# Kernel tuning notes

Measured on AMD Instinct MI355X. Metric: run time of the kernel, lower is better.

## Reference

```python
import jax, jax.numpy as jnp
import numpy as np

LOSS_WEIGHT = 1.0
BIG = 1e9  # finite sentinel for masked-out pixels (avoids inf-grad NaNs)


def setup_inputs() -> dict:
    key = jax.random.key(0)
    k1, k2 = jax.random.split(key)
    B, N, H, W = 4, 6890, 64, 64
    vert2d = jax.random.uniform(k1, (B, N, 2), dtype=jnp.float32) * jnp.array([W, H], jnp.float32)
    mask = jax.random.randint(k2, (B, H, W), 0, 2, dtype=jnp.int32)
    return {"vert2d": vert2d, "mask": mask}


def reference(vert2d, mask):
    B, N, _ = vert2d.shape
    _, H, W = mask.shape
    scale = jnp.array([W, H], vert2d.dtype)
    v = vert2d / scale  # [B,N,2], normalized
    # all pixel coords as (x, y), normalized -- the dense equivalent of torch.where points
    ys, xs = jnp.meshgrid(jnp.arange(H), jnp.arange(W), indexing="ij")
    pts = (jnp.stack([xs.ravel(), ys.ravel()], axis=-1).astype(v.dtype) / scale)  # [HW,2]
    valid = (mask.reshape(B, -1) > 0)  # [B,HW] boolean membership of each pixel
    # pairwise L2 distances: [B,N,HW]
    diff = v[:, :, None, :] - pts[None, None, :, :]
    d = jnp.sqrt(jnp.sum(diff * diff, axis=-1))
    dm = jnp.where(valid[:, None, :], d, BIG)
    # sum over mask points of min over verts  +  sum over verts of min over mask points
    loss = jnp.sum(jnp.min(dm, axis=1) * valid) + jnp.sum(jnp.min(dm, axis=2))
    return LOSS_WEIGHT * loss
```

## Files before the change

### kernel.cpp

```cpp
#include <hip/hip_runtime.h>

#define NB 4
#define NV 6890
#define HW 4096
#define NV4 3445
#define CH4 108
#define CH4P 111
#define NCHUNK 32
#define T2_BPB 54
#define T2_BLOCKS (NB * T2_BPB)
#define T1_BLOCKS (NB * 64)
#define FINF 3.402823466e38f
#define VBIG 1.0e9f
#define PBIG 1.0e18f
#define INV_S (1.0f / 64.0f)

__global__ __launch_bounds__(256) void k_fused(const float* __restrict__ vert,
                                               const int* __restrict__ mask,
                                               float* __restrict__ out) {
    __shared__ __align__(16) char smem[65024];
    int bx = blockIdx.x, tid = threadIdx.x;
    if (bx < T2_BLOCKS) {
        float2* pt = reinterpret_cast<float2*>(smem);
        float*  pr = reinterpret_cast<float*>(smem + 32768);
        float*  sb = reinterpret_cast<float*>(smem + 34816);
        int b = bx / T2_BPB, blk = bx - b * T2_BPB;
        for (int i = tid; i < HW; i += 256) {
            int x = i & 63;
            float fx = (float)x;
            float e = (mask[b * HW + i] > 0) ? fx * fx : PBIG;
            pt[i] = make_float2(-2.f * fx, e);
        }
        int g = tid & 63, rq = tid >> 6;
        int n0 = blk * 128 + 2 * g;
        float4 vp = make_float4(0.f, 0.f, 0.f, 0.f);
        if (n0 < NV)
            vp = reinterpret_cast<const float4*>(vert)[(b * NV + n0) >> 1];
        __syncthreads();
        float vx0 = vp.x, vy0 = vp.y, vx1 = vp.z, vy1 = vp.w;
        float vx20 = vx0 * vx0, vx21 = vx1 * vx1;
        float m0 = FINF, m1 = FINF;
        float fy = (float)(rq * 16);
        for (int y = rq * 16; y < rq * 16 + 16; ++y, fy += 1.f) {
            const float4* row = reinterpret_cast<const float4*>(pt + y * 64);
            float r0 = FINF, r1 = FINF;
            #pragma unroll 8
            for (int j = 0; j < 32; ++j) {
                float4 a = row[j];
                r0 = fminf(r0, fminf(fmaf(a.x, vx0, a.y), fmaf(a.z, vx0, a.w)));
                r1 = fminf(r1, fminf(fmaf(a.x, vx1, a.y), fmaf(a.z, vx1, a.w)));
            }
            float t0 = vy0 - fy, t1 = vy1 - fy;
            m0 = fminf(m0, r0 + fmaf(t0, t0, vx20));
            m1 = fminf(m1, r1 + fmaf(t1, t1, vx21));
        }
        reinterpret_cast<float2*>(pr)[rq * 64 + g] = make_float2(m0, m1);
        __syncthreads();
        float s = 0.f;
        if (tid < 128) {
            float mm = fminf(fminf(pr[tid], pr[128 + tid]),
                             fminf(pr[256 + tid], pr[384 + tid]));
            if (blk * 128 + tid < NV) s = sqrtf(fmaxf(mm, 0.f));
        }
        #pragma unroll
        for (int off = 32; off; off >>= 1) s += __shfl_down(s, off, 64);
        if ((tid & 63) == 0) sb[tid >> 6] = s;
        __syncthreads();
        if (tid == 0) atomicAdd(out, (sb[0] + sb[1] + sb[2] + sb[3]) * INV_S);
    } else {
        float4* v4 = reinterpret_cast<float4*>(smem);
        float*  pr = reinterpret_cast<float*>(smem + 56832);
        int t1i = bx - T2_BLOCKS;
        int x = t1i & 63, b = t1i >> 6;
        const float4* g4 = reinterpret_cast<const float4*>(vert) + b * NV4;
        for (int i = tid; i < NCHUNK * CH4; i += 256) {
            int c = i / CH4;
            float4 w = (i < NV4) ? g4[i] : make_float4(VBIG, 0.f, VBIG, 0.f);
            v4[i + 3 * c] = w;
        }
        __syncthreads();
        int chunk = tid >> 3, ry = tid & 7;
        float fx = (float)x, fm2x = -2.f * fx, fx2 = fx * fx;
        float fm2y[8], m[8];
        #pragma unroll
        for (int k = 0; k < 8; ++k) { fm2y[k] = -2.f * (float)(ry + 8 * k); m[k] = FINF; }
        const float4* cp = v4 + chunk * CH4P;
        #pragma unroll 4
        for (int i = 0; i < CH4; ++i) {
            float4 a = cp[i];
            float vva = fmaf(a.x, a.x, a.y * a.y);
            float vvb = fmaf(a.z, a.z, a.w * a.w);
            float ta = fmaf(fm2x, a.x, vva);
            float tb = fmaf(fm2x, a.z, vvb);
            #pragma unroll
            for (int k = 0; k < 8; ++k) {
                float da = fmaf(fm2y[k], a.y, ta);
                float db = fmaf(fm2y[k], a.w, tb);
                m[k] = fminf(m[k], fminf(da, db));
            }
        }
        #pragma unroll
        for (int k = 0; k < 8; ++k) pr[chunk * 64 + ry + 8 * k] = m[k];
        __syncthreads();
        float e = 0.f;
        if (tid < 64) {
            float mv = pr[tid];
            #pragma unroll
            for (int c = 1; c < NCHUNK; ++c) mv = fminf(mv, pr[c * 64 + tid]);
            if (mask[(b * 64 + tid) * 64 + x] > 0) {
                float fyv = (float)tid;
                e = sqrtf(fmaxf(mv + fmaf(fyv, fyv, fx2), 0.f));
            }
        }
        #pragma unroll
        for (int off = 32; off; off >>= 1) e += __shfl_down(e, off, 64);
        if (tid == 0) atomicAdd(out, e * INV_S);
    }
}

extern "C" void kernel_launch(void* const* d_in, const int* in_sizes, int n_in,
                              void* d_out, int out_size, void* d_ws, size_t ws_size,
                              hipStream_t stream) {
    const float* vert = (const float*)d_in[0];
    const int*   mask = (const int*)d_in[1];
    (void)d_ws; (void)ws_size;
    k_fused<<<T2_BLOCKS + T1_BLOCKS, 256, 0, stream>>>(vert, mask, (float*)d_out);
}
```

Measured before the change: 71.34 us.

## Use 512-thread blocks, register-block 4 verts per thread, share vertex tile across two columns

Blocks double to 512 threads. In the vertex-to-mask branch each thread now handles 4 vertices over 8 rows, and the -2x coefficients are computed in-loop, which halves the per-pixel shared table to scalars. In the mask-to-vertex branch each block covers two pixel columns and reuses one staged vertex tile, which halves global loads and staging per column. The aim is more register reuse and fewer LDS reads per FMA, in exchange for higher register pressure, fewer blocks and an extra barrier.

```diff
diff --git a/kernel.cpp b/kernel.cpp
--- a/kernel.cpp
+++ b/kernel.cpp
@@ -7,87 +7,107 @@
 #define CH4 108
 #define CH4P 111
 #define NCHUNK 32
-#define T2_BPB 54
+#define T2_BPB 27
 #define T2_BLOCKS (NB * T2_BPB)
-#define T1_BLOCKS (NB * 64)
+#define T1_BPB 32
+#define T1_BLOCKS (NB * T1_BPB)
 #define FINF 3.402823466e38f
 #define VBIG 1.0e9f
 #define PBIG 1.0e18f
 #define INV_S (1.0f / 64.0f)
 
-__global__ __launch_bounds__(256) void k_fused(const float* __restrict__ vert,
+__global__ __launch_bounds__(512) void k_fused(const float* __restrict__ vert,
                                                const int* __restrict__ mask,
                                                float* __restrict__ out) {
-    __shared__ __align__(16) char smem[65024];
+    __shared__ __align__(16) char smem[56832];
     int bx = blockIdx.x, tid = threadIdx.x;
     if (bx < T2_BLOCKS) {
-        float2* pt = reinterpret_cast<float2*>(smem);
-        float*  pr = reinterpret_cast<float*>(smem + 32768);
-        float*  sb = reinterpret_cast<float*>(smem + 34816);
+        float* et = reinterpret_cast<float*>(smem);
+        float* pr = reinterpret_cast<float*>(smem + 16384);
+        float* sb = reinterpret_cast<float*>(smem + 24576);
         int b = bx / T2_BPB, blk = bx - b * T2_BPB;
-        for (int i = tid; i < HW; i += 256) {
+        for (int i = tid; i < HW; i += 512) {
             int x = i & 63;
             float fx = (float)x;
-            float e = (mask[b * HW + i] > 0) ? fx * fx : PBIG;
-            pt[i] = make_float2(-2.f * fx, e);
+            et[i] = (mask[b * HW + i] > 0) ? fx * fx : PBIG;
         }
-        int g = tid & 63, rq = tid >> 6;
-        int n0 = blk * 128 + 2 * g;
-        float4 vp = make_float4(0.f, 0.f, 0.f, 0.f);
-        if (n0 < NV)
-            vp = reinterpret_cast<const float4*>(vert)[(b * NV + n0) >> 1];
+        int g = tid & 63, r8 = tid >> 6;
+        int n0 = blk * 256 + 4 * g;
+        const float2* vv2 = reinterpret_cast<const float2*>(vert) + b * NV;
+        float vx[4], vy[4], vx2[4], m[4];
+        #pragma unroll
+        for (int k = 0; k < 4; ++k) {
+            float2 t = (n0 + k < NV) ? vv2[n0 + k] : make_float2(0.f, 0.f);
+            vx[k] = t.x; vy[k] = t.y; vx2[k] = t.x * t.x; m[k] = FINF;
+        }
         __syncthreads();
-        float vx0 = vp.x, vy0 = vp.y, vx1 = vp.z, vy1 = vp.w;
-        float vx20 = vx0 * vx0, vx21 = vx1 * vx1;
-        float m0 = FINF, m1 = FINF;
-        float fy = (float)(rq * 16);
-        for (int y = rq * 16; y < rq * 16 + 16; ++y, fy += 1.f) {
-            const float4* row = reinterpret_cast<const float4*>(pt + y * 64);
-            float r0 = FINF, r1 = FINF;
-            #pragma unroll 8
-            for (int j = 0; j < 32; ++j) {
-                float4 a = row[j];
-                r0 = fminf(r0, fminf(fmaf(a.x, vx0, a.y), fmaf(a.z, vx0, a.w)));
-                r1 = fminf(r1, fminf(fmaf(a.x, vx1, a.y), fmaf(a.z, vx1, a.w)));
+        float fy = (float)(r8 * 8);
+        for (int y = r8 * 8; y < r8 * 8 + 8; ++y, fy += 1.f) {
+            const float4* rowp = reinterpret_cast<const float4*>(et + y * 64);
+            float rm[4] = {FINF, FINF, FINF, FINF};
+            #pragma unroll 4
+            for (int j = 0; j < 16; ++j) {
+                float4 a = rowp[j];
+                float c0 = -8.f * (float)j;
+                float c1 = c0 - 2.f, c2 = c0 - 4.f, c3 = c0 - 6.f;
+                #pragma unroll
+                for (int k = 0; k < 4; ++k) {
+                    float d0 = fmaf(c0, vx[k], a.x);
+                    float d1 = fmaf(c1, vx[k], a.y);
+                    float d2 = fmaf(c2, vx[k], a.z);
+                    float d3 = fmaf(c3, vx[k], a.w);
+                    rm[k] = fminf(rm[k], fminf(d0, d1));
+                    rm[k] = fminf(rm[k], fminf(d2, d3));
+                }
             }
-            float t0 = vy0 - fy, t1 = vy1 - fy;
-            m0 = fminf(m0, r0 + fmaf(t0, t0, vx20));
-            m1 = fminf(m1, r1 + fmaf(t1, t1, vx21));
+            #pragma unroll
+            for (int k = 0; k < 4; ++k) {
+                float ty = vy[k] - fy;
+                m[k] = fminf(m[k], rm[k] + fmaf(ty, ty, vx2[k]));
+            }
         }
-        reinterpret_cast<float2*>(pr)[rq * 64 + g] = make_float2(m0, m1);
+        #pragma unroll
+        for (int k = 0; k < 4; ++k) pr[r8 * 256 + 4 * g + k] = m[k];
         __syncthreads();
         float s = 0.f;
-        if (tid < 128) {
-            float mm = fminf(fminf(pr[tid], pr[128 + tid]),
-                             fminf(pr[256 + tid], pr[384 + tid]));
-            if (blk * 128 + tid < NV) s = sqrtf(fmaxf(mm, 0.f));
+        if (tid < 256) {
+            float mm = pr[tid];
+            #pragma unroll
+            for (int q = 1; q < 8; ++q) mm = fminf(mm, pr[q * 256 + tid]);
+            if (blk * 256 + tid < NV) s = sqrtf(fmaxf(mm, 0.f));
         }
         #pragma unroll
         for (int off = 32; off; off >>= 1) s += __shfl_down(s, off, 64);
         if ((tid & 63) == 0) sb[tid >> 6] = s;
         __syncthreads();
-        if (tid == 0) atomicAdd(out, (sb[0] + sb[1] + sb[2] + sb[3]) * INV_S);
+        if (tid == 0) {
+            float tot = 0.f;
+            #pragma unroll
+            for (int w = 0; w < 8; ++w) tot += sb[w];
+            atomicAdd(out, tot * INV_S);
+        }
     } else {
         float4* v4 = reinterpret_cast<float4*>(smem);
-        float*  pr = reinterpret_cast<float*>(smem + 56832);
         int t1i = bx - T2_BLOCKS;
-        int x = t1i & 63, b = t1i >> 6;
+        int cp = t1i & 31, b = t1i >> 5;
+        int half = tid >> 8, t = tid & 255;
+        int x = 2 * cp + half;
         const float4* g4 = reinterpret_cast<const float4*>(vert) + b * NV4;
-        for (int i = tid; i < NCHUNK * CH4; i += 256) {
+        for (int i = tid; i < NCHUNK * CH4; i += 512) {
             int c = i / CH4;
             float4 w = (i < NV4) ? g4[i] : make_float4(VBIG, 0.f, VBIG, 0.f);
             v4[i + 3 * c] = w;
         }
         __syncthreads();
-        int chunk = tid >> 3, ry = tid & 7;
+        int chunk = t >> 3, ry = t & 7;
         float fx = (float)x, fm2x = -2.f * fx, fx2 = fx * fx;
         float fm2y[8], m[8];
         #pragma unroll
         for (int k = 0; k < 8; ++k) { fm2y[k] = -2.f * (float)(ry + 8 * k); m[k] = FINF; }
-        const float4* cp = v4 + chunk * CH4P;
+        const float4* cpt = v4 + chunk * CH4P;
         #pragma unroll 4
         for (int i = 0; i < CH4; ++i) {
-            float4 a = cp[i];
+            float4 a = cpt[i];
             float vva = fmaf(a.x, a.x, a.y * a.y);
             float vvb = fmaf(a.z, a.z, a.w * a.w);
             float ta = fmaf(fm2x, a.x, vva);
@@ -99,22 +119,24 @@
                 m[k] = fminf(m[k], fminf(da, db));
             }
         }
+        __syncthreads();
+        float* prh = reinterpret_cast<float*>(smem) + half * 2048;
         #pragma unroll
-        for (int k = 0; k < 8; ++k) pr[chunk * 64 + ry + 8 * k] = m[k];
+        for (int k = 0; k < 8; ++k) prh[chunk * 64 + ry + 8 * k] = m[k];
         __syncthreads();
-        float e = 0.f;
-        if (tid < 64) {
-            float mv = pr[tid];
+        if (t < 64) {
+            float mv = prh[t];
             #pragma unroll
-            for (int c = 1; c < NCHUNK; ++c) mv = fminf(mv, pr[c * 64 + tid]);
-            if (mask[(b * 64 + tid) * 64 + x] > 0) {
-                float fyv = (float)tid;
+            for (int c = 1; c < NCHUNK; ++c) mv = fminf(mv, prh[c * 64 + t]);
+            float e = 0.f;
+            if (mask[b * HW + t * 64 + x] > 0) {
+                float fyv = (float)t;
                 e = sqrtf(fmaxf(mv + fmaf(fyv, fyv, fx2), 0.f));
             }
+            #pragma unroll
+            for (int off = 32; off; off >>= 1) e += __shfl_down(e, off, 64);
+            if ((tid & 63) == 0) atomicAdd(out, e * INV_S);
         }
-        #pragma unroll
-        for (int off = 32; off; off >>= 1) e += __shfl_down(e, off, 64);
-        if (tid == 0) atomicAdd(out, e * INV_S);
     }
 }
 
@@ -124,5 +146,5 @@
     const float* vert = (const float*)d_in[0];
     const int*   mask = (const int*)d_in[1];
     (void)d_ws; (void)ws_size;
-    k_fused<<<T2_BLOCKS + T1_BLOCKS, 256, 0, stream>>>(vert, mask, (float*)d_out);
+    k_fused<<<T2_BLOCKS + T1_BLOCKS, 512, 0, stream>>>(vert, mask, (float*)d_out);
 }
```

Measured after the change: 72.10 us. Within noise of the previous version (+1.1%).
